# Optimization experiments

Measured on AMD Instinct MI355X. Metric: run time of the kernel, lower is better.

Reference implementation:

```python
import jax, jax.numpy as jnp
import numpy as np

B, S, H, D = 2, 2048, 16, 64
HID = H * D


def setup_inputs() -> dict:
    key = jax.random.key(0)
    ks = jax.random.split(key, 9)
    s = 1.0 / np.sqrt(HID).astype(np.float32)
    return {
        "hidden_states": jax.random.normal(ks[0], (B, S, HID), dtype=jnp.float32),
        "W_q": jax.random.normal(ks[1], (HID, HID), dtype=jnp.float32) * s,
        "W_k": jax.random.normal(ks[2], (HID, HID), dtype=jnp.float32) * s,
        "W_v": jax.random.normal(ks[3], (HID, HID), dtype=jnp.float32) * s,
        "W_o": jax.random.normal(ks[4], (HID, HID), dtype=jnp.float32) * s,
        "B_q": jax.random.normal(ks[5], (HID,), dtype=jnp.float32) * 0.02,
        "B_k": jax.random.normal(ks[6], (HID,), dtype=jnp.float32) * 0.02,
        "B_v": jax.random.normal(ks[7], (HID,), dtype=jnp.float32) * 0.02,
        "B_o": jax.random.normal(ks[8], (HID,), dtype=jnp.float32) * 0.02,
    }


def _split_heads(x):
    # (B, S, H*D) -> (B, H, S, D)
    b, s, _ = x.shape
    return x.reshape(b, s, H, D).transpose(0, 2, 1, 3)


def reference(hidden_states, W_q, W_k, W_v, W_o, B_q, B_k, B_v, B_o):
    q = _split_heads(hidden_states @ W_q + B_q)
    k = _split_heads(hidden_states @ W_k + B_k)
    v = _split_heads(hidden_states @ W_v + B_v)
    scale = 1.0 / jnp.sqrt(jnp.asarray(D, dtype=q.dtype))
    # (B, H, S, S) attention scores (no mask: original forward never applies it)
    scores = jnp.einsum("bhqd,bhkd->bhqk", q, k) * scale
    weights = jax.nn.softmax(scores, axis=-1)
    attended = jnp.einsum("bhqk,bhkd->bhqd", weights, v)
    # merge heads: (B, H, S, D) -> (B, S, H*D)
    merged = attended.transpose(0, 2, 1, 3).reshape(hidden_states.shape)
    return merged @ W_o + B_o
```

## Files before the change

kernel.cpp:

```cpp
#include <hip/hip_runtime.h>


typedef unsigned short u16;
typedef unsigned int u32;
typedef __attribute__((ext_vector_type(8))) __bf16 bf16x8;
typedef __attribute__((ext_vector_type(4))) float f32x4;
typedef __attribute__((ext_vector_type(16))) float f32x16;

#define MFMA16(a, b, c) __builtin_amdgcn_mfma_f32_16x16x32_bf16((a), (b), (c), 0, 0, 0)
#define MFMA32(a, b, c) __builtin_amdgcn_mfma_f32_32x32x16_bf16((a), (b), (c), 0, 0, 0)

#define GLOAD16(gp, lp)                                                        \
  __builtin_amdgcn_global_load_lds(                                           \
      (const __attribute__((address_space(1))) void*)(gp),                     \
      (__attribute__((address_space(3))) void*)(lp), 16, 0, 0)

static __device__ __forceinline__ u16 f2b(float f) {
  __bf16 b = (__bf16)f;
  return __builtin_bit_cast(u16, b);
}

static __device__ __forceinline__ u32 pk2(float lo, float hi) {
  return (u32)f2b(lo) | ((u32)f2b(hi) << 16);
}

static __device__ __forceinline__ float exp2_fast(float x) {
  float r;
  asm("v_exp_f32 %0, %1" : "=v"(r) : "v"(x));
  return r;
}

static __device__ __forceinline__ bf16x8 ld_glob16(const u16* p) {
  return __builtin_bit_cast(bf16x8, *(const uint4*)p);
}


__global__ void cvt_f32_bf16(const float* __restrict__ in, u16* __restrict__ out, int n4) {
  int i = blockIdx.x * blockDim.x + threadIdx.x;
  if (i >= n4) return;
  float4 v = ((const float4*)in)[i];
  ushort4 o;
  o.x = f2b(v.x); o.y = f2b(v.y); o.z = f2b(v.z); o.w = f2b(v.w);
  ((ushort4*)out)[i] = o;
}

__global__ void wtrans(const float* __restrict__ Wq, const float* __restrict__ Wk,
                       const float* __restrict__ Wv, const float* __restrict__ Wo,
                       u16* __restrict__ wqkvT, u16* __restrict__ woT) {
  __shared__ u16 tile[64][72];
  int z = blockIdx.z;
  const float* W = (z == 0) ? Wq : (z == 1) ? Wk : (z == 2) ? Wv : Wo;
  int n0 = blockIdx.x * 64, k0 = blockIdx.y * 64;
  int t = threadIdx.x;
#pragma unroll
  for (int i = 0; i < 16; ++i) {
    int idx = t + i * 256;
    int r = idx >> 6, c = idx & 63;
    tile[c][r] = f2b(W[(size_t)(k0 + r) * 1024 + n0 + c]);
  }
  __syncthreads();
  u16* dst = (z < 3) ? (wqkvT + (size_t)z * 1024 * 1024) : woT;
#pragma unroll
  for (int i = 0; i < 16; ++i) {
    int idx = t + i * 256;
    int r = idx >> 6, c = idx & 63;
    dst[(size_t)(n0 + r) * 1024 + k0 + c] = tile[r][c];
  }
}

__global__ void bias_concat(const float* __restrict__ Bq, const float* __restrict__ Bk,
                            const float* __restrict__ Bv, float* __restrict__ out) {
  int i = threadIdx.x, z = blockIdx.x;
  out[z * 1024 + i] = (z == 0) ? Bq[i] : (z == 1) ? Bk[i] : Bv[i];
}


template <bool OUT_BF16, bool QSCALE, bool VSPLIT>
__global__ __launch_bounds__(256) void gemm_bt(const u16* __restrict__ A,
                                               const u16* __restrict__ Bt,
                                               const float* __restrict__ bias,
                                               void* __restrict__ out,
                                               u16* __restrict__ vtb2,
                                               int K, int lda, int ldb, int ldo) {
  __shared__ __align__(16) char lA[8192];
  __shared__ __align__(16) char lB[8192];
  int nbx = gridDim.x;
  int f = blockIdx.x + nbx * blockIdx.y;
  int cpx = (nbx * gridDim.y) >> 3;
  int v = (f & 7) * cpx + (f >> 3);
  int m0 = (v % nbx) * 128, n0 = (v / nbx) * 128;
  int t = threadIdx.x, w = t >> 6, lane = t & 63, g = lane >> 4, ln = lane & 15;
  int wr = w >> 1, wc = w & 1;
  f32x4 acc[4][4] = {};
  int nkt = K >> 5;
  for (int kt = 0; kt < nkt; ++kt) {
    __syncthreads();
#pragma unroll
    for (int s = 0; s < 2; ++s) {
      int row = s * 64 + (t >> 2), c = t & 3, gg = c ^ ((row >> 1) & 3);
      GLOAD16(A + (size_t)(m0 + row) * lda + kt * 32 + gg * 8, lA + s * 4096 + w * 1024);
    }
#pragma unroll
    for (int s = 0; s < 2; ++s) {
      int row = s * 64 + (t >> 2), c = t & 3, gg = c ^ ((row >> 1) & 3);
      GLOAD16(Bt + (size_t)(n0 + row) * ldb + kt * 32 + gg * 8, lB + s * 4096 + w * 1024);
    }
    __syncthreads();
    bf16x8 af[4], bf_[4];
#pragma unroll
    for (int mi = 0; mi < 4; ++mi) {
      int row = wr * 64 + mi * 16 + ln;
      af[mi] = __builtin_bit_cast(
          bf16x8, *(const uint4*)(lA + row * 64 + ((g ^ ((row >> 1) & 3)) << 4)));
    }
#pragma unroll
    for (int ni = 0; ni < 4; ++ni) {
      int row = wc * 64 + ni * 16 + ln;
      bf_[ni] = __builtin_bit_cast(
          bf16x8, *(const uint4*)(lB + row * 64 + ((g ^ ((row >> 1) & 3)) << 4)));
    }
#pragma unroll
    for (int mi = 0; mi < 4; ++mi)
#pragma unroll
      for (int ni = 0; ni < 4; ++ni)
        acc[mi][ni] = MFMA16(af[mi], bf_[ni], acc[mi][ni]);
  }
#pragma unroll
  for (int mi = 0; mi < 4; ++mi) {
#pragma unroll
    for (int ni = 0; ni < 4; ++ni) {
      int n = n0 + wc * 64 + ni * 16 + ln;
      float bs = bias[n];
      float scale = QSCALE ? ((n < 1024) ? 0.18033688011f : 1.0f) : 1.0f;
      float vv[4];
#pragma unroll
      for (int r = 0; r < 4; ++r) vv[r] = (acc[mi][ni][r] + bs) * scale;
      int mbase = m0 + wr * 64 + mi * 16 + g * 4;
      if (VSPLIT && n >= 2048) {
        int bh = ((m0 >> 11) << 4) | ((n >> 6) & 15);
        int sloc = mbase & 2047;
        sloc = (sloc & ~15) | ((sloc & 4) << 1) | ((sloc & 8) >> 1);
        size_t vbase = (size_t)(bh * 64 + (n & 63)) * 2048 + sloc;
        *(uint2*)(vtb2 + vbase) = make_uint2(pk2(vv[0], vv[1]), pk2(vv[2], vv[3]));
      } else if (OUT_BF16) {
#pragma unroll
        for (int r = 0; r < 4; ++r)
          ((u16*)out)[(size_t)(mbase + r) * ldo + n] = f2b(vv[r]);
      } else {
#pragma unroll
        for (int r = 0; r < 4; ++r)
          ((float*)out)[(size_t)(mbase + r) * ldo + n] = vv[r];
      }
    }
  }
}

__global__ __launch_bounds__(256, 2) void attn(const u16* __restrict__ qkv,
                                               const u16* __restrict__ vt,
                                               u16* __restrict__ att) {
  __shared__ __align__(16) char lds[32768];

  int f = blockIdx.x + 16 * blockIdx.y;
  int v = (f & 7) * 64 + (f >> 3);
  int qt = v & 15, bh = v >> 4;
  int b = bh >> 4, h = bh & 15;

  int t = threadIdx.x, w = t >> 6, lane = t & 63;
  int col = lane & 31, hi = lane >> 5, a7 = lane & 7;

  int qrow = qt * 128 + w * 32 + col;
  const u16* qp = qkv + (size_t)(b * 2048 + qrow) * 3072 + h * 64;
  bf16x8 qf[4];
#pragma unroll
  for (int kst = 0; kst < 4; ++kst) qf[kst] = ld_glob16(qp + kst * 16 + hi * 8);

  int gg = (lane & 7) ^ (lane >> 3);
  const u16* kp0 = qkv + (size_t)(b * 2048 + 16 * w + (lane >> 3)) * 3072 + 1024 + h * 64 + gg * 8;
  const u16* vp0 = vt + (size_t)(bh * 64 + 16 * w + (lane >> 3)) * 2048 + gg * 8;

#define STAGE_KV(bufoff, itv)                                                  \
  {                                                                            \
    const u16* ka = kp0 + (size_t)(itv) * 196608;                              \
    const u16* va = vp0 + (size_t)(itv) * 64;                                  \
    GLOAD16(ka, lds + (bufoff) + 2048 * w);                                    \
    GLOAD16(ka + 24576, lds + (bufoff) + 2048 * w + 1024);                     \
    GLOAD16(va, lds + (bufoff) + 8192 + 2048 * w);                             \
    GLOAD16(va + 16384, lds + (bufoff) + 8192 + 2048 * w + 1024);              \
  }

  f32x16 O0 = {}, O1 = {};
  float lsum = 0.f;

  STAGE_KV(0, 0);

  for (int it = 0; it < 32; ++it) {
    const int bufo = (it & 1) * 16384;
    if (it < 31) {
      STAGE_KV(((it + 1) & 1) * 16384, it + 1);
      asm volatile("s_waitcnt vmcnt(4)" ::: "memory");
    } else {
      asm volatile("s_waitcnt vmcnt(0)" ::: "memory");
    }
    __builtin_amdgcn_s_barrier();
    asm volatile("" ::: "memory");

    const char* lK = lds + bufo;
    const char* lV = lds + bufo + 8192;

    f32x16 s0 = {}, s1 = {};
    __builtin_amdgcn_s_setprio(1);
#pragma unroll
    for (int kst = 0; kst < 4; ++kst) {
      int slot = ((2 * kst + hi) ^ a7) << 4;
      bf16x8 k0 = *(const bf16x8*)(lK + col * 128 + slot);
      bf16x8 k1 = *(const bf16x8*)(lK + (32 + col) * 128 + slot);
      s0 = MFMA32(k0, qf[kst], s0);
      s1 = MFMA32(k1, qf[kst], s1);
    }
    __builtin_amdgcn_s_setprio(0);

    float a0 = 0.f, a1 = 0.f, a2 = 0.f, a3 = 0.f;
#pragma unroll
    for (int r = 0; r < 16; r += 4) {
      float p0 = exp2_fast(s0[r + 0]); s0[r + 0] = p0; a0 += p0;
      float p1 = exp2_fast(s0[r + 1]); s0[r + 1] = p1; a1 += p1;
      float p2 = exp2_fast(s0[r + 2]); s0[r + 2] = p2; a2 += p2;
      float p3 = exp2_fast(s0[r + 3]); s0[r + 3] = p3; a3 += p3;
    }
#pragma unroll
    for (int r = 0; r < 16; r += 4) {
      float p0 = exp2_fast(s1[r + 0]); s1[r + 0] = p0; a0 += p0;
      float p1 = exp2_fast(s1[r + 1]); s1[r + 1] = p1; a1 += p1;
      float p2 = exp2_fast(s1[r + 2]); s1[r + 2] = p2; a2 += p2;
      float p3 = exp2_fast(s1[r + 3]); s1[r + 3] = p3; a3 += p3;
    }
    float ps = (a0 + a1) + (a2 + a3);
    ps += __shfl_xor(ps, 32);
    lsum += ps;

    u32 cpk[2][8];
#pragma unroll
    for (int rp = 0; rp < 8; ++rp) {
      cpk[0][rp] = pk2(s0[2 * rp], s0[2 * rp + 1]);
      cpk[1][rp] = pk2(s1[2 * rp], s1[2 * rp + 1]);
    }

    __builtin_amdgcn_s_setprio(1);
#pragma unroll
    for (int ks = 0; ks < 4; ++ks) {
      const int tt = ks >> 1, base = (ks & 1) * 4;
      union { u32 u[4]; bf16x8 v8; } B;
      B.u[0] = cpk[tt][base + 0];
      B.u[1] = cpk[tt][base + 1];
      B.u[2] = cpk[tt][base + 2];
      B.u[3] = cpk[tt][base + 3];
      int slot = ((2 * ks + hi) ^ a7) << 4;
      bf16x8 v0 = *(const bf16x8*)(lV + col * 128 + slot);
      bf16x8 v1 = *(const bf16x8*)(lV + (32 + col) * 128 + slot);
      O0 = MFMA32(v0, B.v8, O0);
      O1 = MFMA32(v1, B.v8, O1);
    }
    __builtin_amdgcn_s_setprio(0);

    asm volatile("" ::: "memory");
    __builtin_amdgcn_s_barrier();
    asm volatile("" ::: "memory");
  }

  float inv = 1.0f / lsum;
  char* tp = lds + w * 4096;
#pragma unroll
  for (int dt = 0; dt < 2; ++dt) {
#pragma unroll
    for (int g2 = 0; g2 < 4; ++g2) {
      float a0, a1, b0, b1;
      if (dt == 0) {
        a0 = O0[4 * g2 + 0]; a1 = O0[4 * g2 + 1];
        b0 = O0[4 * g2 + 2]; b1 = O0[4 * g2 + 3];
      } else {
        a0 = O1[4 * g2 + 0]; a1 = O1[4 * g2 + 1];
        b0 = O1[4 * g2 + 2]; b1 = O1[4 * g2 + 3];
      }
      u32 w0 = pk2(a0 * inv, a1 * inv);
      u32 w1 = pk2(b0 * inv, b1 * inv);
      int dq0 = 16 * dt + 4 * g2 + 2 * hi;
      int slot = dq0 ^ ((col & 7) << 2);
      *(uint2*)(tp + col * 128 + slot * 4) = make_uint2(w0, w1);
    }
  }
  asm volatile("s_waitcnt lgkmcnt(0)" ::: "memory");
  __builtin_amdgcn_sched_barrier(0);
  int q_r = lane >> 1, pr = lane & 1;
  size_t orow = (size_t)(b * 2048 + qt * 128 + w * 32 + q_r) * 1024 + h * 64;
#pragma unroll
  for (int j = 0; j < 4; ++j) {
    int dqb = 16 * pr + 4 * j;
    int slot = dqb ^ ((q_r & 7) << 2);
    uint4 val = *(const uint4*)(tp + q_r * 128 + slot * 4);
    *(uint4*)(att + orow + 2 * dqb) = val;
  }
#undef STAGE_KV
}


extern "C" void kernel_launch(void* const* d_in, const int* in_sizes, int n_in,
                              void* d_out, int out_size, void* d_ws, size_t ws_size,
                              hipStream_t stream) {
  const float* hidden = (const float*)d_in[0];
  const float* Wq = (const float*)d_in[1];
  const float* Wk = (const float*)d_in[2];
  const float* Wv = (const float*)d_in[3];
  const float* Wo = (const float*)d_in[4];
  const float* Bq = (const float*)d_in[5];
  const float* Bk = (const float*)d_in[6];
  const float* Bv = (const float*)d_in[7];
  const float* Bo = (const float*)d_in[8];

  char* ws = (char*)d_ws;
  u16* hiddenB = (u16*)(ws + 0);
  u16* wqkvT   = (u16*)(ws + 8388608);
  u16* woT     = (u16*)(ws + 14680064);
  float* biasQ = (float*)(ws + 16777216);
  u16* qkv     = (u16*)(ws + 16789504);
  u16* vtb     = (u16*)(ws + 41955328);
  u16* att     = hiddenB;

  cvt_f32_bf16<<<4096, 256, 0, stream>>>(hidden, hiddenB, 1048576);
  wtrans<<<dim3(16, 16, 4), 256, 0, stream>>>(Wq, Wk, Wv, Wo, wqkvT, woT);
  bias_concat<<<3, 1024, 0, stream>>>(Bq, Bk, Bv, biasQ);
  gemm_bt<true, true, true><<<dim3(32, 24), 256, 0, stream>>>(
      hiddenB, wqkvT, biasQ, qkv, vtb, 1024, 1024, 1024, 3072);
  attn<<<dim3(16, 32), 256, 0, stream>>>(qkv, vtb, att);
  gemm_bt<false, false, false><<<dim3(32, 8), 256, 0, stream>>>(
      att, woT, Bo, d_out, nullptr, 1024, 1024, 1024, 1024);
}
```

Before: 133.1 us.

## Double attention query tile per wave to reuse K/V LDS loads

Each wave now processes 64 query rows (two 32-row sub-tiles) instead of 32, so each block covers 256 queries and the grid halves to 256 blocks. K and V fragments read from LDS are reused across both query sub-tiles, halving LDS and global K/V traffic per query. In exchange, register pressure roughly doubles (launch bounds drop to one block per SM), and with only 256 blocks on a GPU with 256 CUs there is less latency hiding and occupancy.

```diff
diff --git a/kernel.cpp b/kernel.cpp
--- a/kernel.cpp
+++ b/kernel.cpp
@@ -155,24 +155,27 @@
   }
 }
 
-__global__ __launch_bounds__(256, 2) void attn(const u16* __restrict__ qkv,
+__global__ __launch_bounds__(256, 1) void attn(const u16* __restrict__ qkv,
                                                const u16* __restrict__ vt,
                                                u16* __restrict__ att) {
   __shared__ __align__(16) char lds[32768];
 
-  int f = blockIdx.x + 16 * blockIdx.y;
-  int v = (f & 7) * 64 + (f >> 3);
-  int qt = v & 15, bh = v >> 4;
+  int f = blockIdx.x + 8 * blockIdx.y;
+  int v = (f & 7) * 32 + (f >> 3);
+  int qt = v & 7, bh = v >> 3;
   int b = bh >> 4, h = bh & 15;
 
   int t = threadIdx.x, w = t >> 6, lane = t & 63;
   int col = lane & 31, hi = lane >> 5, a7 = lane & 7;
 
-  int qrow = qt * 128 + w * 32 + col;
-  const u16* qp = qkv + (size_t)(b * 2048 + qrow) * 3072 + h * 64;
-  bf16x8 qf[4];
-#pragma unroll
-  for (int kst = 0; kst < 4; ++kst) qf[kst] = ld_glob16(qp + kst * 16 + hi * 8);
+  int qbase = qt * 256 + w * 64;
+  const u16* qp = qkv + (size_t)(b * 2048 + qbase + col) * 3072 + h * 64;
+  bf16x8 qf0[4], qf1[4];
+#pragma unroll
+  for (int kst = 0; kst < 4; ++kst) {
+    qf0[kst] = ld_glob16(qp + kst * 16 + hi * 8);
+    qf1[kst] = ld_glob16(qp + 32 * 3072 + kst * 16 + hi * 8);
+  }
 
   int gg = (lane & 7) ^ (lane >> 3);
   const u16* kp0 = qkv + (size_t)(b * 2048 + 16 * w + (lane >> 3)) * 3072 + 1024 + h * 64 + gg * 8;
@@ -188,8 +191,8 @@
     GLOAD16(va + 16384, lds + (bufoff) + 8192 + 2048 * w + 1024);              \
   }
 
-  f32x16 O0 = {}, O1 = {};
-  float lsum = 0.f;
+  f32x16 O00 = {}, O01 = {}, O10 = {}, O11 = {};
+  float lsum0 = 0.f, lsum1 = 0.f;
 
   STAGE_KV(0, 0);
 
@@ -207,58 +210,77 @@
     const char* lK = lds + bufo;
     const char* lV = lds + bufo + 8192;
 
-    f32x16 s0 = {}, s1 = {};
+    f32x16 s00 = {}, s01 = {}, s10 = {}, s11 = {};
     __builtin_amdgcn_s_setprio(1);
 #pragma unroll
     for (int kst = 0; kst < 4; ++kst) {
       int slot = ((2 * kst + hi) ^ a7) << 4;
       bf16x8 k0 = *(const bf16x8*)(lK + col * 128 + slot);
       bf16x8 k1 = *(const bf16x8*)(lK + (32 + col) * 128 + slot);
-      s0 = MFMA32(k0, qf[kst], s0);
-      s1 = MFMA32(k1, qf[kst], s1);
+      s00 = MFMA32(k0, qf0[kst], s00);
+      s01 = MFMA32(k1, qf0[kst], s01);
+      s10 = MFMA32(k0, qf1[kst], s10);
+      s11 = MFMA32(k1, qf1[kst], s11);
     }
     __builtin_amdgcn_s_setprio(0);
 
     float a0 = 0.f, a1 = 0.f, a2 = 0.f, a3 = 0.f;
+    float b0 = 0.f, b1 = 0.f, b2 = 0.f, b3 = 0.f;
 #pragma unroll
     for (int r = 0; r < 16; r += 4) {
-      float p0 = exp2_fast(s0[r + 0]); s0[r + 0] = p0; a0 += p0;
-      float p1 = exp2_fast(s0[r + 1]); s0[r + 1] = p1; a1 += p1;
-      float p2 = exp2_fast(s0[r + 2]); s0[r + 2] = p2; a2 += p2;
-      float p3 = exp2_fast(s0[r + 3]); s0[r + 3] = p3; a3 += p3;
+      float p0 = exp2_fast(s00[r + 0]); s00[r + 0] = p0; a0 += p0;
+      float p1 = exp2_fast(s00[r + 1]); s00[r + 1] = p1; a1 += p1;
+      float p2 = exp2_fast(s00[r + 2]); s00[r + 2] = p2; a2 += p2;
+      float p3 = exp2_fast(s00[r + 3]); s00[r + 3] = p3; a3 += p3;
+      float q0 = exp2_fast(s10[r + 0]); s10[r + 0] = q0; b0 += q0;
+      float q1 = exp2_fast(s10[r + 1]); s10[r + 1] = q1; b1 += q1;
+      float q2 = exp2_fast(s10[r + 2]); s10[r + 2] = q2; b2 += q2;
+      float q3 = exp2_fast(s10[r + 3]); s10[r + 3] = q3; b3 += q3;
     }
 #pragma unroll
     for (int r = 0; r < 16; r += 4) {
-      float p0 = exp2_fast(s1[r + 0]); s1[r + 0] = p0; a0 += p0;
-      float p1 = exp2_fast(s1[r + 1]); s1[r + 1] = p1; a1 += p1;
-      float p2 = exp2_fast(s1[r + 2]); s1[r + 2] = p2; a2 += p2;
-      float p3 = exp2_fast(s1[r + 3]); s1[r + 3] = p3; a3 += p3;
-    }
-    float ps = (a0 + a1) + (a2 + a3);
-    ps += __shfl_xor(ps, 32);
-    lsum += ps;
-
-    u32 cpk[2][8];
+      float p0 = exp2_fast(s01[r + 0]); s01[r + 0] = p0; a0 += p0;
+      float p1 = exp2_fast(s01[r + 1]); s01[r + 1] = p1; a1 += p1;
+      float p2 = exp2_fast(s01[r + 2]); s01[r + 2] = p2; a2 += p2;
+      float p3 = exp2_fast(s01[r + 3]); s01[r + 3] = p3; a3 += p3;
+      float q0 = exp2_fast(s11[r + 0]); s11[r + 0] = q0; b0 += q0;
+      float q1 = exp2_fast(s11[r + 1]); s11[r + 1] = q1; b1 += q1;
+      float q2 = exp2_fast(s11[r + 2]); s11[r + 2] = q2; b2 += q2;
+      float q3 = exp2_fast(s11[r + 3]); s11[r + 3] = q3; b3 += q3;
+    }
+    float ps0 = (a0 + a1) + (a2 + a3);
+    float ps1 = (b0 + b1) + (b2 + b3);
+    ps0 += __shfl_xor(ps0, 32);
+    ps1 += __shfl_xor(ps1, 32);
+    lsum0 += ps0;
+    lsum1 += ps1;
+
+    u32 cpk0[2][8], cpk1[2][8];
 #pragma unroll
     for (int rp = 0; rp < 8; ++rp) {
-      cpk[0][rp] = pk2(s0[2 * rp], s0[2 * rp + 1]);
-      cpk[1][rp] = pk2(s1[2 * rp], s1[2 * rp + 1]);
+      cpk0[0][rp] = pk2(s00[2 * rp], s00[2 * rp + 1]);
+      cpk0[1][rp] = pk2(s01[2 * rp], s01[2 * rp + 1]);
+      cpk1[0][rp] = pk2(s10[2 * rp], s10[2 * rp + 1]);
+      cpk1[1][rp] = pk2(s11[2 * rp], s11[2 * rp + 1]);
     }
 
     __builtin_amdgcn_s_setprio(1);
 #pragma unroll
     for (int ks = 0; ks < 4; ++ks) {
       const int tt = ks >> 1, base = (ks & 1) * 4;
-      union { u32 u[4]; bf16x8 v8; } B;
-      B.u[0] = cpk[tt][base + 0];
-      B.u[1] = cpk[tt][base + 1];
-      B.u[2] = cpk[tt][base + 2];
-      B.u[3] = cpk[tt][base + 3];
+      union { u32 u[4]; bf16x8 v8; } B0, B1;
+#pragma unroll
+      for (int i = 0; i < 4; ++i) {
+        B0.u[i] = cpk0[tt][base + i];
+        B1.u[i] = cpk1[tt][base + i];
+      }
       int slot = ((2 * ks + hi) ^ a7) << 4;
       bf16x8 v0 = *(const bf16x8*)(lV + col * 128 + slot);
       bf16x8 v1 = *(const bf16x8*)(lV + (32 + col) * 128 + slot);
-      O0 = MFMA32(v0, B.v8, O0);
-      O1 = MFMA32(v1, B.v8, O1);
+      O00 = MFMA32(v0, B0.v8, O00);
+      O01 = MFMA32(v1, B0.v8, O01);
+      O10 = MFMA32(v0, B1.v8, O10);
+      O11 = MFMA32(v1, B1.v8, O11);
     }
     __builtin_amdgcn_s_setprio(0);
 
@@ -267,37 +289,55 @@
     asm volatile("" ::: "memory");
   }
 
-  float inv = 1.0f / lsum;
-  char* tp = lds + w * 4096;
-#pragma unroll
-  for (int dt = 0; dt < 2; ++dt) {
-#pragma unroll
-    for (int g2 = 0; g2 < 4; ++g2) {
-      float a0, a1, b0, b1;
-      if (dt == 0) {
-        a0 = O0[4 * g2 + 0]; a1 = O0[4 * g2 + 1];
-        b0 = O0[4 * g2 + 2]; b1 = O0[4 * g2 + 3];
-      } else {
-        a0 = O1[4 * g2 + 0]; a1 = O1[4 * g2 + 1];
-        b0 = O1[4 * g2 + 2]; b1 = O1[4 * g2 + 3];
+  char* tpw = lds + w * 8192;
+#pragma unroll
+  for (int j = 0; j < 2; ++j) {
+    float inv = (j == 0) ? (1.0f / lsum0) : (1.0f / lsum1);
+    char* tp = tpw + j * 4096;
+#pragma unroll
+    for (int dt = 0; dt < 2; ++dt) {
+#pragma unroll
+      for (int g2 = 0; g2 < 4; ++g2) {
+        float a0, a1, b0, b1;
+        if (j == 0) {
+          if (dt == 0) {
+            a0 = O00[4 * g2 + 0]; a1 = O00[4 * g2 + 1];
+            b0 = O00[4 * g2 + 2]; b1 = O00[4 * g2 + 3];
+          } else {
+            a0 = O01[4 * g2 + 0]; a1 = O01[4 * g2 + 1];
+            b0 = O01[4 * g2 + 2]; b1 = O01[4 * g2 + 3];
+          }
+        } else {
+          if (dt == 0) {
+            a0 = O10[4 * g2 + 0]; a1 = O10[4 * g2 + 1];
+            b0 = O10[4 * g2 + 2]; b1 = O10[4 * g2 + 3];
+          } else {
+            a0 = O11[4 * g2 + 0]; a1 = O11[4 * g2 + 1];
+            b0 = O11[4 * g2 + 2]; b1 = O11[4 * g2 + 3];
+          }
+        }
+        u32 w0 = pk2(a0 * inv, a1 * inv);
+        u32 w1 = pk2(b0 * inv, b1 * inv);
+        int dq0 = 16 * dt + 4 * g2 + 2 * hi;
+        int slot = dq0 ^ ((col & 7) << 2);
+        *(uint2*)(tp + col * 128 + slot * 4) = make_uint2(w0, w1);
       }
-      u32 w0 = pk2(a0 * inv, a1 * inv);
-      u32 w1 = pk2(b0 * inv, b1 * inv);
-      int dq0 = 16 * dt + 4 * g2 + 2 * hi;
-      int slot = dq0 ^ ((col & 7) << 2);
-      *(uint2*)(tp + col * 128 + slot * 4) = make_uint2(w0, w1);
     }
   }
   asm volatile("s_waitcnt lgkmcnt(0)" ::: "memory");
   __builtin_amdgcn_sched_barrier(0);
   int q_r = lane >> 1, pr = lane & 1;
-  size_t orow = (size_t)(b * 2048 + qt * 128 + w * 32 + q_r) * 1024 + h * 64;
-#pragma unroll
-  for (int j = 0; j < 4; ++j) {
-    int dqb = 16 * pr + 4 * j;
-    int slot = dqb ^ ((q_r & 7) << 2);
-    uint4 val = *(const uint4*)(tp + q_r * 128 + slot * 4);
-    *(uint4*)(att + orow + 2 * dqb) = val;
+#pragma unroll
+  for (int j = 0; j < 2; ++j) {
+    char* tp = tpw + j * 4096;
+    size_t orow = (size_t)(b * 2048 + qbase + j * 32 + q_r) * 1024 + h * 64;
+#pragma unroll
+    for (int jj = 0; jj < 4; ++jj) {
+      int dqb = 16 * pr + 4 * jj;
+      int slot = dqb ^ ((q_r & 7) << 2);
+      uint4 val = *(const uint4*)(tp + q_r * 128 + slot * 4);
+      *(uint4*)(att + orow + 2 * dqb) = val;
+    }
   }
 #undef STAGE_KV
 }
@@ -330,7 +370,7 @@
   bias_concat<<<3, 1024, 0, stream>>>(Bq, Bk, Bv, biasQ);
   gemm_bt<true, true, true><<<dim3(32, 24), 256, 0, stream>>>(
       hiddenB, wqkvT, biasQ, qkv, vtb, 1024, 1024, 1024, 3072);
-  attn<<<dim3(16, 32), 256, 0, stream>>>(qkv, vtb, att);
+  attn<<<dim3(8, 32), 256, 0, stream>>>(qkv, vtb, att);
   gemm_bt<false, false, false><<<dim3(32, 8), 256, 0, stream>>>(
       att, woT, Bo, d_out, nullptr, 1024, 1024, 1024, 1024);
 }
```

New measurement: 143.3 us. 1.08x slower.
